# Kernel optimization log

Measured on AMD Instinct MI355X. Metric: run time of the kernel, lower is better.

## Reference

```python
import jax, jax.numpy as jnp
import numpy as np

B, S, D = 8, 1025, 768
H, KV, HD = 12, 4, 64
GH, GW = 32, 32
EPS = 1e-6


def setup_inputs() -> dict:
    key = jax.random.key(0)
    ks = jax.random.split(key, 6)
    sc = 0.02
    hidden_states = jax.random.normal(ks[0], (B, S, D), jnp.float32)
    attention_mask = jnp.ones((B, S), dtype=bool)
    image_pos_ids = jnp.broadcast_to(jnp.arange(S, dtype=jnp.int32), (B, S))
    return dict(
        hidden_states=hidden_states,
        attention_mask=attention_mask,
        image_pos_ids=image_pos_ids,
        grid_h=GH,
        grid_w=GW,
        Wq=jax.random.normal(ks[1], (D, H * HD), jnp.float32) * sc,
        Wk=jax.random.normal(ks[2], (D, KV * HD), jnp.float32) * sc,
        Wv=jax.random.normal(ks[3], (D, KV * HD), jnp.float32) * sc,
        Wo=jax.random.normal(ks[4], (H * HD, D), jnp.float32) * sc,
        q_norm_w=jnp.ones((HD,), jnp.float32),
        k_norm_w=jnp.ones((HD,), jnp.float32),
    )


def _rmsnorm(x, w, eps=EPS):
    return x * jax.lax.rsqrt(jnp.mean(x * x, axis=-1, keepdims=True) + eps) * w


def _rotate(x, cos, sin):
    # x: [B, h, P, HD]; cos/sin: [B, P, HD//2]. Pairs are adjacent (view_as_complex).
    hd = x.shape[-1]
    xr = x.reshape(*x.shape[:-1], hd // 2, 2)
    x0, x1 = xr[..., 0], xr[..., 1]
    c, s = cos[:, None], sin[:, None]  # broadcast over heads
    o0 = x0 * c - x1 * s
    o1 = x0 * s + x1 * c
    return jnp.stack([o0, o1], axis=-1).reshape(x.shape)


def reference(hidden_states, attention_mask, image_pos_ids, grid_h, grid_w,
              Wq, Wk, Wv, Wo, q_norm_w, k_norm_w):
    b, s, d = hidden_states.shape
    hd = q_norm_w.shape[0]
    h = Wq.shape[1] // hd
    kv = Wk.shape[1] // hd
    n_rep = h // kv
    scale = hd ** -0.5

    q = _rmsnorm((hidden_states @ Wq).reshape(b, s, h, hd), q_norm_w).transpose(0, 2, 1, 3)
    k = _rmsnorm((hidden_states @ Wk).reshape(b, s, kv, hd), k_norm_w).transpose(0, 2, 1, 3)
    v = (hidden_states @ Wv).reshape(b, s, kv, hd).transpose(0, 2, 1, 3)

    # 2D RoPE on patch tokens only (CLS token at position 0 excluded)
    ids = image_pos_ids[:, 1:]
    hi = (ids // grid_w) % grid_h
    wi = ids % grid_w
    half, quarter = hd // 2, hd // 4
    inv_freq = 1.0 / (10000.0 ** (jnp.arange(quarter, dtype=jnp.float32) * 2.0 / half))
    ang = jnp.concatenate([hi[..., None] * inv_freq, wi[..., None] * inv_freq], axis=-1)  # [B,P,HD/2]
    cos, sin = jnp.cos(ang), jnp.sin(ang)
    q = jnp.concatenate([q[:, :, :1], _rotate(q[:, :, 1:], cos, sin)], axis=2)
    k = jnp.concatenate([k[:, :, :1], _rotate(k[:, :, 1:], cos, sin)], axis=2)

    # GQA: repeat_interleave kv heads to match query heads
    kr = jnp.repeat(k, n_rep, axis=1)
    vr = jnp.repeat(v, n_rep, axis=1)

    scores = jnp.einsum('bhqd,bhkd->bhqk', q, kr) * scale
    add = jnp.where(attention_mask, 0.0, jnp.finfo(jnp.float32).min)[:, None, None, :]
    scores = scores + add
    attn = jax.nn.softmax(scores.astype(jnp.float32), axis=-1).astype(q.dtype)
    out = jnp.einsum('bhqk,bhkd->bqhd', attn, vr).reshape(b, s, h * hd)
    return (out @ Wo, attn)
```

## Files before the change

kernel.cpp:

```cpp
#include <hip/hip_runtime.h>

#define B_ 8
#define S_ 1025
#define D_ 768
#define H_ 12
#define KV_ 4
#define HD_ 64
#define NREP 3
#define SCALE_ 0.125f
#define EPS_ 1e-6f
#define SKP 1088
#define PST 1096
#define QBLK 16
#define NQT 65
#define DYNLDS 35072

typedef __attribute__((ext_vector_type(8))) short bf16x8;
typedef __attribute__((ext_vector_type(4))) float f32x4;

__device__ __forceinline__ unsigned short f2bf(float f) {
  unsigned int u = __builtin_bit_cast(unsigned int, f);
  return (unsigned short)((u + 0x7FFFu + ((u >> 16) & 1u)) >> 16);
}
__device__ __forceinline__ unsigned int pk2(float a, float b) {
  return (unsigned int)f2bf(a) | ((unsigned int)f2bf(b) << 16);
}
__device__ __forceinline__ float bf2f(unsigned short u) {
  return __builtin_bit_cast(float, (unsigned int)u << 16);
}
__device__ __forceinline__ unsigned int cvtpk(float a, float b) {
  unsigned int r;
  asm("v_cvt_pk_bf16_f32 %0, %1, %2" : "=v"(r) : "v"(a), "v"(b));
  return r;
}

__device__ __forceinline__ void barrier_lgkm() {
  __builtin_amdgcn_sched_barrier(0);
  asm volatile("s_waitcnt lgkmcnt(0)" ::: "memory");
  __builtin_amdgcn_s_barrier();
  __builtin_amdgcn_sched_barrier(0);
}

__global__ __launch_bounds__(256) void cast_x_kernel(const float* __restrict__ x,
                                                     unsigned short* __restrict__ xb, int n4) {
  int i = blockIdx.x * 256 + threadIdx.x;
  if (i >= n4) return;
  f32x4 v = *(const f32x4*)(x + (size_t)i * 4);
  uint2 o;
  o.x = pk2(v[0], v[1]);
  o.y = pk2(v[2], v[3]);
  *(uint2*)(xb + (size_t)i * 4) = o;
}

__global__ __launch_bounds__(256) void cast_wqkv_kernel(const float* __restrict__ Wq,
    const float* __restrict__ Wk, const float* __restrict__ Wv,
    unsigned short* __restrict__ WT) {
  int idx = blockIdx.x * 256 + threadIdx.x;
  int n = idx / D_, k = idx % D_;
  float v;
  if (n < 768)       v = Wq[(size_t)k * 768 + n];
  else if (n < 1024) v = Wk[(size_t)k * 256 + (n - 768)];
  else               v = Wv[(size_t)k * 256 + (n - 1024)];
  WT[idx] = f2bf(v);
}

__global__ __launch_bounds__(256) void cast_wo_kernel(const float* __restrict__ Wo,
                                                      unsigned short* __restrict__ WT) {
  int idx = blockIdx.x * 256 + threadIdx.x;
  int n = idx / D_, k = idx % D_;
  WT[idx] = f2bf(Wo[(size_t)k * D_ + n]);
}

#define BM 128
#define BN 128
#define BK 32
#define LSTR 40
__global__ __launch_bounds__(256) void gemm_bt(const unsigned short* __restrict__ A,
    const unsigned short* __restrict__ BT, float* __restrict__ C, int M, int N, int K) {
  __shared__ unsigned short As[BM * LSTR];
  __shared__ unsigned short Bs[BN * LSTR];
  const int nMt = (M + BM - 1) / BM;
  const int tm = blockIdx.x % nMt;
  const int tn = blockIdx.x / nMt;
  const int row0 = tm * BM, col0 = tn * BN;
  const int tid = threadIdx.x;
  const int l = tid & 63, w = tid >> 6;
  const int wr = (w >> 1) * 64, wc = (w & 1) * 64;
  const int lr = l & 15, lk = (l >> 4) * 8;
  f32x4 acc[4][4] = {};
  for (int kt = 0; kt < K; kt += BK) {
    __syncthreads();
#pragma unroll
    for (int i = 0; i < 2; ++i) {
      int c = tid + i * 256;
      int r = c >> 2;
      int ce = (c & 3) * 8;
      int gr = row0 + r; gr = gr < M ? gr : M - 1;
      bf16x8 va = *(const bf16x8*)(A + (size_t)gr * K + kt + ce);
      *(bf16x8*)&As[r * LSTR + ce] = va;
      bf16x8 vb = *(const bf16x8*)(BT + (size_t)(col0 + r) * K + kt + ce);
      *(bf16x8*)&Bs[r * LSTR + ce] = vb;
    }
    __syncthreads();
    bf16x8 af[4], bfr[4];
#pragma unroll
    for (int m = 0; m < 4; ++m)
      af[m] = *(const bf16x8*)&As[(wr + m * 16 + lr) * LSTR + lk];
#pragma unroll
    for (int n = 0; n < 4; ++n)
      bfr[n] = *(const bf16x8*)&Bs[(wc + n * 16 + lr) * LSTR + lk];
#pragma unroll
    for (int m = 0; m < 4; ++m)
#pragma unroll
      for (int n = 0; n < 4; ++n)
        acc[m][n] = __builtin_amdgcn_mfma_f32_16x16x32_bf16(af[m], bfr[n], acc[m][n], 0, 0, 0);
  }
  const int orow = (l >> 4) * 4;
#pragma unroll
  for (int m = 0; m < 4; ++m)
#pragma unroll
    for (int n = 0; n < 4; ++n)
#pragma unroll
      for (int r = 0; r < 4; ++r) {
        int row = row0 + wr + m * 16 + orow + r;
        int col = col0 + wc + n * 16 + lr;
        if (row < M) C[(size_t)row * N + col] = acc[m][n][r];
      }
}

__global__ __launch_bounds__(256) void qkv_epilogue(const float* __restrict__ QKV,
    const int* __restrict__ pos_ids, const int* __restrict__ ghp, const int* __restrict__ gwp,
    const float* __restrict__ qw, const float* __restrict__ kw,
    unsigned short* __restrict__ Qb, unsigned short* __restrict__ Kb,
    unsigned short* __restrict__ Vt) {
  if (blockIdx.x < B_ * KV_) {
    unsigned short* vp = Vt + (size_t)blockIdx.x * 64 * SKP;
    for (int idx = threadIdx.x; idx < 64 * 63; idx += 256) {
      int d = idx / 63, s = S_ + idx % 63;
      vp[d * SKP + s] = 0;
    }
  }
  int tok = blockIdx.x * 4 + (threadIdx.x >> 6);
  int l = threadIdx.x & 63;
  if (tok >= B_ * S_) return;
  int b = tok / S_, s = tok % S_;
  const float* rowp = QKV + (size_t)tok * 1280;
  bool rot = (s > 0);
  float cs = 1.f, sn = 0.f;
  if (rot) {
    int gh = ghp[0], gw = gwp[0];
    int pos = pos_ids[tok];
    int hi = (pos / gw) % gh;
    int wi = pos % gw;
    int pi = l >> 1;
    int j = pi < 16 ? pi : pi - 16;
    float invf = exp2f(-(float)j * (13.287712379549449f / 16.f));
    float ang = (pi < 16 ? (float)hi : (float)wi) * invf;
    cs = cosf(ang); sn = sinf(ang);
  }
#pragma unroll
  for (int h = 0; h < H_; ++h) {
    float x = rowp[h * 64 + l];
    float ss = x * x;
    for (int off = 32; off; off >>= 1) ss += __shfl_xor(ss, off);
    float xn = x * rsqrtf(ss * (1.f / 64.f) + EPS_) * qw[l];
    float o = xn;
    if (rot) {
      float p = __shfl_xor(xn, 1);
      o = (l & 1) ? (p * sn + xn * cs) : (xn * cs - p * sn);
    }
    o *= SCALE_;
    Qb[((size_t)(b * H_ + h) * S_ + s) * 64 + l] = f2bf(o);
  }
#pragma unroll
  for (int h = 0; h < KV_; ++h) {
    float x = rowp[768 + h * 64 + l];
    float ss = x * x;
    for (int off = 32; off; off >>= 1) ss += __shfl_xor(ss, off);
    float xn = x * rsqrtf(ss * (1.f / 64.f) + EPS_) * kw[l];
    float o = xn;
    if (rot) {
      float p = __shfl_xor(xn, 1);
      o = (l & 1) ? (p * sn + xn * cs) : (xn * cs - p * sn);
    }
    Kb[((size_t)(b * KV_ + h) * S_ + s) * 64 + l] = f2bf(o);
    float v = rowp[1024 + h * 64 + l];
    Vt[((size_t)(b * KV_ + h) * 64 + l) * SKP + s] = f2bf(v);
  }
}

__global__ __launch_bounds__(512, 4) void attn_kernel(const unsigned short* __restrict__ Qb,
    const unsigned short* __restrict__ Kb, const unsigned short* __restrict__ Vt,
    unsigned short* __restrict__ ctx, float* __restrict__ attn_out) {
  extern __shared__ unsigned short Psh[];
  __shared__ float partial[4][64][4];
  __shared__ float red[8][16];
  __shared__ unsigned short ctxs[16][64];
  int bid = blockIdx.x;
  int swz = (bid & 7) * 780 + (bid >> 3);
  int qt = swz % NQT;
  int h = (swz / NQT) % H_;
  int b = swz / (NQT * H_);
  int kvh = h / NREP;
  int q0 = qt * QBLK;
  int tid = threadIdx.x;
  int l = tid & 63, w = tid >> 6;
  int lr = l & 15, lk = (l >> 4) * 8;

  const unsigned short* Qbase = Qb + (size_t)(b * H_ + h) * S_ * 64;
  const unsigned short* Kbase = Kb + (size_t)(b * KV_ + kvh) * S_ * 64;
  const unsigned short* Vbase = Vt + (size_t)(b * KV_ + kvh) * 64 * SKP;

  int qrow = q0 + lr; if (qrow >= S_) qrow = S_ - 1;
  bf16x8 qf0 = *(const bf16x8*)(Qbase + (size_t)qrow * 64 + lk);
  bf16x8 qf1 = *(const bf16x8*)(Qbase + (size_t)qrow * 64 + 32 + lk);

  float psum = 0.f;
  {
    const int g4 = (l >> 4) * 4;
    const int kb = (w < 4) ? w * 144 : 576 + (w - 4) * 128;
#pragma unroll
    for (int j = 0; j < 9; ++j) {
      if (w < 4 || j < 8) {
        int kr = kb + j * 16 + lr; if (kr > 1024) kr = 1024;
        const unsigned short* kp = Kbase + (size_t)kr * 64;
        bf16x8 kf0 = *(const bf16x8*)(kp + lk);
        bf16x8 kf1 = *(const bf16x8*)(kp + 32 + lk);
        f32x4 acc = {};
        acc = __builtin_amdgcn_mfma_f32_16x16x32_bf16(kf0, qf0, acc, 0, 0, 0);
        acc = __builtin_amdgcn_mfma_f32_16x16x32_bf16(kf1, qf1, acc, 0, 0, 0);
        int key0 = kb + j * 16 + g4;
        float e0 = (key0     <= 1024) ? __expf(acc[0]) : 0.f;
        float e1 = (key0 + 1 <= 1024) ? __expf(acc[1]) : 0.f;
        float e2 = (key0 + 2 <= 1024) ? __expf(acc[2]) : 0.f;
        float e3 = (key0 + 3 <= 1024) ? __expf(acc[3]) : 0.f;
        psum += (e0 + e1) + (e2 + e3);
        uint2 pw; pw.x = cvtpk(e0, e1); pw.y = cvtpk(e2, e3);
        *(uint2*)&Psh[(size_t)lr * PST + key0] = pw;
      }
    }
  }
  psum += __shfl_xor(psum, 16);
  psum += __shfl_xor(psum, 32);
  if (l < 16) red[w][l] = psum;
  barrier_lgkm();

  float invq;
  {
    float s = 0.f;
#pragma unroll
    for (int j2 = 0; j2 < 8; ++j2) s += red[j2][lr];
    invq = 1.f / s;
  }

  f32x4 accv = {};
  {
    const int d0 = (w & 3) * 16;
    const int kh = (w >> 2) * 544;
    const int prow = lr * PST + kh;
    const unsigned short* vb = Vbase + (size_t)(d0 + lr) * SKP + kh;
#pragma unroll 4
    for (int kc = 0; kc < 17; ++kc) {
      bf16x8 pa = *(const bf16x8*)&Psh[prow + kc * 32 + lk];
      bf16x8 vf = *(const bf16x8*)(vb + kc * 32 + lk);
      accv = __builtin_amdgcn_mfma_f32_16x16x32_bf16(pa, vf, accv, 0, 0, 0);
    }
  }
  if (w >= 4) *(f32x4*)partial[w - 4][l] = accv;
  barrier_lgkm();
  if (w < 4) {
    accv += *(const f32x4*)partial[w][l];
    int rowb = (l >> 4) * 4;
    int d0 = (w & 3) * 16;
#pragma unroll
    for (int r = 0; r < 4; ++r) {
      float iv = __shfl(invq, rowb + r);
      ctxs[rowb + r][d0 + lr] = f2bf(accv[r] * iv);
    }
  }
  barrier_lgkm();
  {
    int t = 2 * w + (l >> 5);
    int q = q0 + t;
    if (q < S_) {
      unsigned int u = *(const unsigned int*)&ctxs[t][2 * (l & 31)];
      *(unsigned int*)(ctx + (size_t)(b * S_ + q) * 768 + h * 64 + 2 * (l & 31)) = u;
    }
  }

#pragma unroll
  for (int rr = 0; rr < 2; ++rr) {
    int rowi = w + rr * 8;
    int q = q0 + rowi;
    if (q < S_) {
      float rinv = __shfl(invq, rowi);
      const unsigned short* Prow = Psh + (size_t)rowi * PST;
      float* gout = attn_out + ((size_t)(b * H_ + h) * S_ + q) * S_;
      int a = (4 - (q & 3)) & 3;
      int nx4 = (1025 - a) >> 2;
      int tl = 1025 - a - 4 * nx4;
      if (l < a) gout[l] = bf2f(Prow[l]) * rinv;
      if (l < tl) { int idx = a + 4 * nx4 + l; gout[idx] = bf2f(Prow[idx]) * rinv; }
      if (a == 0) {
#pragma unroll
        for (int c = 0; c < 4; ++c) {
          int ch = c * 64 + l;
          if (ch < nx4) {
            uint2 u = *(const uint2*)&Prow[4 * ch];
            f32x4 o;
            o[0] = __builtin_bit_cast(float, u.x << 16) * rinv;
            o[1] = __builtin_bit_cast(float, u.x & 0xffff0000u) * rinv;
            o[2] = __builtin_bit_cast(float, u.y << 16) * rinv;
            o[3] = __builtin_bit_cast(float, u.y & 0xffff0000u) * rinv;
            *(f32x4*)(gout + 4 * ch) = o;
          }
        }
      } else if (a == 2) {
#pragma unroll
        for (int c = 0; c < 4; ++c) {
          int ch = c * 64 + l;
          if (ch < nx4) {
            unsigned int u0 = *(const unsigned int*)&Prow[4 * ch + 2];
            unsigned int u1 = *(const unsigned int*)&Prow[4 * ch + 4];
            f32x4 o;
            o[0] = __builtin_bit_cast(float, u0 << 16) * rinv;
            o[1] = __builtin_bit_cast(float, u0 & 0xffff0000u) * rinv;
            o[2] = __builtin_bit_cast(float, u1 << 16) * rinv;
            o[3] = __builtin_bit_cast(float, u1 & 0xffff0000u) * rinv;
            *(f32x4*)(gout + 2 + 4 * ch) = o;
          }
        }
      } else if (a == 1) {
#pragma unroll
        for (int c = 0; c < 4; ++c) {
          int ch = c * 64 + l;
          if (ch < nx4) {
            uint2 d01 = *(const uint2*)&Prow[4 * ch];
            unsigned int d2 = *(const unsigned int*)&Prow[4 * ch + 4];
            unsigned int u0 = __builtin_amdgcn_alignbit(d01.y, d01.x, 16);
            unsigned int u1 = __builtin_amdgcn_alignbit(d2, d01.y, 16);
            f32x4 o;
            o[0] = __builtin_bit_cast(float, u0 << 16) * rinv;
            o[1] = __builtin_bit_cast(float, u0 & 0xffff0000u) * rinv;
            o[2] = __builtin_bit_cast(float, u1 << 16) * rinv;
            o[3] = __builtin_bit_cast(float, u1 & 0xffff0000u) * rinv;
            *(f32x4*)(gout + 1 + 4 * ch) = o;
          }
        }
      } else {
#pragma unroll
        for (int c = 0; c < 4; ++c) {
          int ch = c * 64 + l;
          if (ch < nx4) {
            unsigned int d0 = *(const unsigned int*)&Prow[4 * ch + 2];
            uint2 d12 = *(const uint2*)&Prow[4 * ch + 4];
            unsigned int u0 = __builtin_amdgcn_alignbit(d12.x, d0, 16);
            unsigned int u1 = __builtin_amdgcn_alignbit(d12.y, d12.x, 16);
            f32x4 o;
            o[0] = __builtin_bit_cast(float, u0 << 16) * rinv;
            o[1] = __builtin_bit_cast(float, u0 & 0xffff0000u) * rinv;
            o[2] = __builtin_bit_cast(float, u1 << 16) * rinv;
            o[3] = __builtin_bit_cast(float, u1 & 0xffff0000u) * rinv;
            *(f32x4*)(gout + 3 + 4 * ch) = o;
          }
        }
      }
    }
  }
}

extern "C" void kernel_launch(void* const* d_in, const int* in_sizes, int n_in,
                              void* d_out, int out_size, void* d_ws, size_t ws_size,
                              hipStream_t stream) {
  const float* hidden = (const float*)d_in[0];
  const int* pos_ids = (const int*)d_in[2];
  const int* ghp = (const int*)d_in[3];
  const int* gwp = (const int*)d_in[4];
  const float* Wq = (const float*)d_in[5];
  const float* Wk = (const float*)d_in[6];
  const float* Wv = (const float*)d_in[7];
  const float* Wo = (const float*)d_in[8];
  const float* qnw = (const float*)d_in[9];
  const float* knw = (const float*)d_in[10];

  char* ws = (char*)d_ws;
  unsigned short* Xb    = (unsigned short*)ws;
  unsigned short* WqkvT = (unsigned short*)(ws + 12595200);
  unsigned short* WoT   = (unsigned short*)(ws + 14561280);
  float*          QKV   = (float*)(ws + 15740928);
  unsigned short* ctx   = (unsigned short*)(ws + 15740928);
  unsigned short* Qb    = (unsigned short*)(ws + 57724928);
  unsigned short* Kb    = (unsigned short*)(ws + 70320128);
  unsigned short* Vt    = (unsigned short*)(ws + 74518528);

  float* out0 = (float*)d_out;
  float* attn_out = out0 + (size_t)B_ * S_ * D_;

  cast_x_kernel<<<6150, 256, 0, stream>>>(hidden, Xb, 1574400);
  cast_wqkv_kernel<<<3840, 256, 0, stream>>>(Wq, Wk, Wv, WqkvT);
  cast_wo_kernel<<<2304, 256, 0, stream>>>(Wo, WoT);

  gemm_bt<<<65 * 10, 256, 0, stream>>>(Xb, WqkvT, QKV, B_ * S_, 1280, D_);

  qkv_epilogue<<<2050, 256, 0, stream>>>(QKV, pos_ids, ghp, gwp, qnw, knw, Qb, Kb, Vt);

  hipFuncSetAttribute((const void*)attn_kernel,
                      hipFuncAttributeMaxDynamicSharedMemorySize, DYNLDS);
  attn_kernel<<<B_ * H_ * NQT, 512, DYNLDS, stream>>>(Qb, Kb, Vt, ctx, attn_out);

  gemm_bt<<<65 * 6, 256, 0, stream>>>(ctx, WoT, out0, B_ * S_, D_, D_);
}
```

Before: 340.3 us.

## Split attention into core kernel and separate aligned probability expansion kernel

The attention kernel now writes unnormalized bf16 probabilities and per-row inverse sums to a padded workspace buffer. A second kernel reads them back, normalizes them and writes the fp32 attention matrix with 16-byte aligned vector stores, handling per-row misalignment. The aim is to take the large, misaligned fp32 attention store out of the MMA-heavy kernel. In exchange it adds an extra round trip of the bf16 probability matrix through global memory and depends on a large workspace being available, falling back to the old kernel otherwise.

```diff
diff --git a/kernel.cpp b/kernel.cpp
--- a/kernel.cpp
+++ b/kernel.cpp
@@ -11,9 +11,11 @@
 #define EPS_ 1e-6f
 #define SKP 1088
 #define PST 1096
+#define PGS 1088
 #define QBLK 16
 #define NQT 65
 #define DYNLDS 35072
+#define NROWS (B_ * H_ * S_)
 
 typedef __attribute__((ext_vector_type(8))) short bf16x8;
 typedef __attribute__((ext_vector_type(4))) float f32x4;
@@ -189,9 +191,10 @@
   }
 }
 
-__global__ __launch_bounds__(512, 4) void attn_kernel(const unsigned short* __restrict__ Qb,
+__global__ __launch_bounds__(512, 4) void attn_core_kernel(const unsigned short* __restrict__ Qb,
     const unsigned short* __restrict__ Kb, const unsigned short* __restrict__ Vt,
-    unsigned short* __restrict__ ctx, float* __restrict__ attn_out) {
+    unsigned short* __restrict__ ctx, unsigned short* __restrict__ Pg,
+    float* __restrict__ invg) {
   extern __shared__ unsigned short Psh[];
   __shared__ float partial[4][64][4];
   __shared__ float red[8][16];
@@ -210,6 +213,7 @@
   const unsigned short* Qbase = Qb + (size_t)(b * H_ + h) * S_ * 64;
   const unsigned short* Kbase = Kb + (size_t)(b * KV_ + kvh) * S_ * 64;
   const unsigned short* Vbase = Vt + (size_t)(b * KV_ + kvh) * 64 * SKP;
+  const int rowbase = (b * H_ + h) * S_;
 
   int qrow = q0 + lr; if (qrow >= S_) qrow = S_ - 1;
   bf16x8 qf0 = *(const bf16x8*)(Qbase + (size_t)qrow * 64 + lk);
@@ -253,6 +257,181 @@
     invq = 1.f / s;
   }
 
+  if (w == 0 && l < 16) {
+    int q = q0 + l;
+    if (q < S_) invg[rowbase + q] = invq;
+  }
+
+#pragma unroll
+  for (int rr = 0; rr < 2; ++rr) {
+    int rowi = w + rr * 8;
+    int q = q0 + rowi;
+    if (q < S_) {
+      const unsigned short* Prow = Psh + (size_t)rowi * PST;
+      unsigned short* gp = Pg + (size_t)(rowbase + q) * PGS;
+      bf16x8 v0 = *(const bf16x8*)&Prow[l * 8];
+      bf16x8 v1 = *(const bf16x8*)&Prow[512 + l * 8];
+      *(bf16x8*)&gp[l * 8] = v0;
+      *(bf16x8*)&gp[512 + l * 8] = v1;
+      if (l < 8) {
+        bf16x8 v2 = *(const bf16x8*)&Prow[1024 + l * 8];
+        *(bf16x8*)&gp[1024 + l * 8] = v2;
+      }
+    }
+  }
+
+  f32x4 accv = {};
+  {
+    const int d0 = (w & 3) * 16;
+    const int kh = (w >> 2) * 544;
+    const int prow = lr * PST + kh;
+    const unsigned short* vb = Vbase + (size_t)(d0 + lr) * SKP + kh;
+#pragma unroll 4
+    for (int kc = 0; kc < 17; ++kc) {
+      bf16x8 pa = *(const bf16x8*)&Psh[prow + kc * 32 + lk];
+      bf16x8 vf = *(const bf16x8*)(vb + kc * 32 + lk);
+      accv = __builtin_amdgcn_mfma_f32_16x16x32_bf16(pa, vf, accv, 0, 0, 0);
+    }
+  }
+  if (w >= 4) *(f32x4*)partial[w - 4][l] = accv;
+  barrier_lgkm();
+  if (w < 4) {
+    accv += *(const f32x4*)partial[w][l];
+    int rowb = (l >> 4) * 4;
+    int d0 = (w & 3) * 16;
+#pragma unroll
+    for (int r = 0; r < 4; ++r) {
+      float iv = __shfl(invq, rowb + r);
+      ctxs[rowb + r][d0 + lr] = f2bf(accv[r] * iv);
+    }
+  }
+  barrier_lgkm();
+  {
+    int t = 2 * w + (l >> 5);
+    int q = q0 + t;
+    if (q < S_) {
+      unsigned int u = *(const unsigned int*)&ctxs[t][2 * (l & 31)];
+      *(unsigned int*)(ctx + (size_t)(b * S_ + q) * 768 + h * 64 + 2 * (l & 31)) = u;
+    }
+  }
+}
+
+__global__ __launch_bounds__(256) void attn_expand_kernel(const unsigned short* __restrict__ Pg,
+    const float* __restrict__ invg, float* __restrict__ attn_out) {
+  int t = threadIdx.x;
+  for (int R = blockIdx.x; R < NROWS; R += gridDim.x) {
+    const unsigned short* Prow = Pg + (size_t)R * PGS;
+    float* gout = attn_out + (size_t)R * 1025;
+    float rinv = invg[R];
+    int a = (4 - (R & 3)) & 3;
+    int nx4 = (1025 - a) >> 2;
+    int tl = 1025 - a - 4 * nx4;
+    if (t < a) gout[t] = bf2f(Prow[t]) * rinv;
+    if (t < tl) { int idx = a + 4 * nx4 + t; gout[idx] = bf2f(Prow[idx]) * rinv; }
+    int ch = t;
+    if (ch < nx4) {
+      f32x4 o;
+      if (a == 0) {
+        uint2 u = *(const uint2*)&Prow[4 * ch];
+        o[0] = __builtin_bit_cast(float, u.x << 16) * rinv;
+        o[1] = __builtin_bit_cast(float, u.x & 0xffff0000u) * rinv;
+        o[2] = __builtin_bit_cast(float, u.y << 16) * rinv;
+        o[3] = __builtin_bit_cast(float, u.y & 0xffff0000u) * rinv;
+      } else if (a == 2) {
+        unsigned int u0 = *(const unsigned int*)&Prow[4 * ch + 2];
+        unsigned int u1 = *(const unsigned int*)&Prow[4 * ch + 4];
+        o[0] = __builtin_bit_cast(float, u0 << 16) * rinv;
+        o[1] = __builtin_bit_cast(float, u0 & 0xffff0000u) * rinv;
+        o[2] = __builtin_bit_cast(float, u1 << 16) * rinv;
+        o[3] = __builtin_bit_cast(float, u1 & 0xffff0000u) * rinv;
+      } else if (a == 1) {
+        uint2 d01 = *(const uint2*)&Prow[4 * ch];
+        unsigned int d2 = *(const unsigned int*)&Prow[4 * ch + 4];
+        unsigned int u0 = __builtin_amdgcn_alignbit(d01.y, d01.x, 16);
+        unsigned int u1 = __builtin_amdgcn_alignbit(d2, d01.y, 16);
+        o[0] = __builtin_bit_cast(float, u0 << 16) * rinv;
+        o[1] = __builtin_bit_cast(float, u0 & 0xffff0000u) * rinv;
+        o[2] = __builtin_bit_cast(float, u1 << 16) * rinv;
+        o[3] = __builtin_bit_cast(float, u1 & 0xffff0000u) * rinv;
+      } else {
+        unsigned int d0 = *(const unsigned int*)&Prow[4 * ch + 2];
+        uint2 d12 = *(const uint2*)&Prow[4 * ch + 4];
+        unsigned int u0 = __builtin_amdgcn_alignbit(d12.x, d0, 16);
+        unsigned int u1 = __builtin_amdgcn_alignbit(d12.y, d12.x, 16);
+        o[0] = __builtin_bit_cast(float, u0 << 16) * rinv;
+        o[1] = __builtin_bit_cast(float, u0 & 0xffff0000u) * rinv;
+        o[2] = __builtin_bit_cast(float, u1 << 16) * rinv;
+        o[3] = __builtin_bit_cast(float, u1 & 0xffff0000u) * rinv;
+      }
+      *(f32x4*)(gout + a + 4 * ch) = o;
+    }
+  }
+}
+
+__global__ __launch_bounds__(512, 4) void attn_kernel(const unsigned short* __restrict__ Qb,
+    const unsigned short* __restrict__ Kb, const unsigned short* __restrict__ Vt,
+    unsigned short* __restrict__ ctx, float* __restrict__ attn_out) {
+  extern __shared__ unsigned short Psh[];
+  __shared__ float partial[4][64][4];
+  __shared__ float red[8][16];
+  __shared__ unsigned short ctxs[16][64];
+  int bid = blockIdx.x;
+  int swz = (bid & 7) * 780 + (bid >> 3);
+  int qt = swz % NQT;
+  int h = (swz / NQT) % H_;
+  int b = swz / (NQT * H_);
+  int kvh = h / NREP;
+  int q0 = qt * QBLK;
+  int tid = threadIdx.x;
+  int l = tid & 63, w = tid >> 6;
+  int lr = l & 15, lk = (l >> 4) * 8;
+
+  const unsigned short* Qbase = Qb + (size_t)(b * H_ + h) * S_ * 64;
+  const unsigned short* Kbase = Kb + (size_t)(b * KV_ + kvh) * S_ * 64;
+  const unsigned short* Vbase = Vt + (size_t)(b * KV_ + kvh) * 64 * SKP;
+
+  int qrow = q0 + lr; if (qrow >= S_) qrow = S_ - 1;
+  bf16x8 qf0 = *(const bf16x8*)(Qbase + (size_t)qrow * 64 + lk);
+  bf16x8 qf1 = *(const bf16x8*)(Qbase + (size_t)qrow * 64 + 32 + lk);
+
+  float psum = 0.f;
+  {
+    const int g4 = (l >> 4) * 4;
+    const int kb = (w < 4) ? w * 144 : 576 + (w - 4) * 128;
+#pragma unroll
+    for (int j = 0; j < 9; ++j) {
+      if (w < 4 || j < 8) {
+        int kr = kb + j * 16 + lr; if (kr > 1024) kr = 1024;
+        const unsigned short* kp = Kbase + (size_t)kr * 64;
+        bf16x8 kf0 = *(const bf16x8*)(kp + lk);
+        bf16x8 kf1 = *(const bf16x8*)(kp + 32 + lk);
+        f32x4 acc = {};
+        acc = __builtin_amdgcn_mfma_f32_16x16x32_bf16(kf0, qf0, acc, 0, 0, 0);
+        acc = __builtin_amdgcn_mfma_f32_16x16x32_bf16(kf1, qf1, acc, 0, 0, 0);
+        int key0 = kb + j * 16 + g4;
+        float e0 = (key0     <= 1024) ? __expf(acc[0]) : 0.f;
+        float e1 = (key0 + 1 <= 1024) ? __expf(acc[1]) : 0.f;
+        float e2 = (key0 + 2 <= 1024) ? __expf(acc[2]) : 0.f;
+        float e3 = (key0 + 3 <= 1024) ? __expf(acc[3]) : 0.f;
+        psum += (e0 + e1) + (e2 + e3);
+        uint2 pw; pw.x = cvtpk(e0, e1); pw.y = cvtpk(e2, e3);
+        *(uint2*)&Psh[(size_t)lr * PST + key0] = pw;
+      }
+    }
+  }
+  psum += __shfl_xor(psum, 16);
+  psum += __shfl_xor(psum, 32);
+  if (l < 16) red[w][l] = psum;
+  barrier_lgkm();
+
+  float invq;
+  {
+    float s = 0.f;
+#pragma unroll
+    for (int j2 = 0; j2 < 8; ++j2) s += red[j2][lr];
+    invq = 1.f / s;
+  }
+
   f32x4 accv = {};
   {
     const int d0 = (w & 3) * 16;
@@ -392,6 +571,9 @@
   unsigned short* Qb    = (unsigned short*)(ws + 57724928);
   unsigned short* Kb    = (unsigned short*)(ws + 70320128);
   unsigned short* Vt    = (unsigned short*)(ws + 74518528);
+  unsigned short* Pg    = (unsigned short*)(ws + 78974976);
+  float*          invg  = (float*)(ws + 293093376);
+  const size_t NEED_SPLIT = 293486976;
 
   float* out0 = (float*)d_out;
   float* attn_out = out0 + (size_t)B_ * S_ * D_;
@@ -404,9 +586,16 @@
 
   qkv_epilogue<<<2050, 256, 0, stream>>>(QKV, pos_ids, ghp, gwp, qnw, knw, Qb, Kb, Vt);
 
-  hipFuncSetAttribute((const void*)attn_kernel,
-                      hipFuncAttributeMaxDynamicSharedMemorySize, DYNLDS);
-  attn_kernel<<<B_ * H_ * NQT, 512, DYNLDS, stream>>>(Qb, Kb, Vt, ctx, attn_out);
+  if (ws_size >= NEED_SPLIT) {
+    hipFuncSetAttribute((const void*)attn_core_kernel,
+                        hipFuncAttributeMaxDynamicSharedMemorySize, DYNLDS);
+    attn_core_kernel<<<B_ * H_ * NQT, 512, DYNLDS, stream>>>(Qb, Kb, Vt, ctx, Pg, invg);
+    attn_expand_kernel<<<4096, 256, 0, stream>>>(Pg, invg, attn_out);
+  } else {
+    hipFuncSetAttribute((const void*)attn_kernel,
+                        hipFuncAttributeMaxDynamicSharedMemorySize, DYNLDS);
+    attn_kernel<<<B_ * H_ * NQT, 512, DYNLDS, stream>>>(Qb, Kb, Vt, ctx, attn_out);
+  }
 
   gemm_bt<<<65 * 6, 256, 0, stream>>>(ctx, WoT, out0, B_ * S_, D_, D_);
 }
```

After: 496.5 us. 1.46x slower.
